# Kernel tuning notes

Measured on AMD Instinct MI355X. Metric: run time of the kernel, lower is better.

Reference implementation:

```python
import jax, jax.numpy as jnp
import numpy as np

S = 5            # num_species
B = 1_000_000    # batch (proteins)
D = 32           # input_dim == hidden_dim (hard-coded 32 in forward)
EPS = 1e-5       # torch BatchNorm1d default eps
BRANCH_WEIGHT = 0.92


def setup_inputs() -> dict:
    key = jax.random.key(0)
    ks = jax.random.split(key, 20)
    f32 = jnp.float32
    inp = {
        "network_feat": jax.random.normal(ks[0], (B, D), f32),
        "species_ids": jax.random.randint(ks[1], (B,), 0, S),
        # per-species params, stacked along species axis. Weights stored [in, out]
        # (transpose of torch nn.Linear layout) so y = x @ W + b.
        "W1": jax.random.normal(ks[2], (S, D, D), f32) * 0.1,
        "b1": jax.random.normal(ks[3], (S, D), f32) * 0.1,
        "bn1_gamma": jax.random.uniform(ks[4], (S, D), f32, 0.5, 1.5),
        "bn1_beta": jax.random.normal(ks[5], (S, D), f32) * 0.1,
        "bn1_mean": jax.random.normal(ks[6], (S, D), f32) * 0.1,
        "bn1_var": jax.random.uniform(ks[7], (S, D), f32, 0.5, 1.5),
        "W2": jax.random.normal(ks[8], (S, D, D), f32) * 0.1,
        "b2": jax.random.normal(ks[9], (S, D), f32) * 0.1,
        "bn2_gamma": jax.random.uniform(ks[10], (S, D), f32, 0.5, 1.5),
        "bn2_beta": jax.random.normal(ks[11], (S, D), f32) * 0.1,
        "bn2_mean": jax.random.normal(ks[12], (S, D), f32) * 0.1,
        "bn2_var": jax.random.uniform(ks[13], (S, D), f32, 0.5, 1.5),
        "Wsc": jax.random.normal(ks[14], (S, D, D), f32) * 0.1,
        "bsc": jax.random.normal(ks[15], (S, D), f32) * 0.1,
        "Wsh": jax.random.normal(ks[16], (D, D), f32) * 0.1,
        "bsh": jax.random.normal(ks[17], (D,), f32) * 0.1,
    }
    return inp


def _bn(h, gamma, beta, mean, var):
    # BatchNorm1d in eval mode: running-stat normalization + affine.
    return (h - mean) * jax.lax.rsqrt(var + EPS) * gamma + beta


def reference(network_feat, species_ids, W1, b1, bn1_gamma, bn1_beta, bn1_mean,
              bn1_var, W2, b2, bn2_gamma, bn2_beta, bn2_mean, bn2_var,
              Wsc, bsc, Wsh, bsh):
    # Eval mode: dropout = identity, BN uses running stats.
    # Instead of gather/scatter per species, compute each species' tiny MLP on the
    # full batch and select with the species mask (same math; dense & fusible).
    x = network_feat
    out = jnp.zeros_like(x)
    for s in range(S):  # small fixed expert count
        shortcut = x @ Wsc[s] + bsc[s]
        h = jax.nn.relu(x @ W1[s] + b1[s])
        h = _bn(h, bn1_gamma[s], bn1_beta[s], bn1_mean[s], bn1_var[s])
        h = jax.nn.relu(h @ W2[s] + b2[s] + shortcut)
        h = _bn(h, bn2_gamma[s], bn2_beta[s], bn2_mean[s], bn2_var[s])
        mask = (species_ids == s)[:, None]  # [B, 1]
        out = jnp.where(mask, h, out)
    out = jax.nn.relu(out @ Wsh + bsh)  # shared MLP (dropout inactive)
    return out * BRANCH_WEIGHT
```

## Files before the change

### kernel.cpp

```cpp
#include <hip/hip_runtime.h>


#define EPSBN 1e-5f
#define TPB 256
#define NBLKMAX 768
#define WROWS 1024
#define MAXSLOT 1184
#define MAXTILE 37

typedef __attribute__((ext_vector_type(8))) short bf16x8;
typedef __attribute__((ext_vector_type(16))) float f32x16;
typedef __attribute__((ext_vector_type(4))) unsigned u32x4;

union FU { unsigned u[4]; bf16x8 v; u32x4 q; };

static __device__ __forceinline__ unsigned pkbf(float lo, float hi) {
    unsigned r;
    asm("v_cvt_pk_bf16_f32 %0, %1, %2" : "=v"(r) : "v"(lo), "v"(hi));
    return r;
}

__global__ void k_pre(unsigned* __restrict__ wfrag, float* __restrict__ bconst,
                      const float* __restrict__ W1, const float* __restrict__ b1,
                      const float* __restrict__ g1, const float* __restrict__ be1,
                      const float* __restrict__ mu1, const float* __restrict__ va1,
                      const float* __restrict__ W2, const float* __restrict__ b2,
                      const float* __restrict__ g2, const float* __restrict__ be2,
                      const float* __restrict__ mu2, const float* __restrict__ va2,
                      const float* __restrict__ Wsc, const float* __restrict__ bsc,
                      const float* __restrict__ Wsh, const float* __restrict__ bsh) {
    if (blockIdx.x < 40) {
        const int i = blockIdx.x * 256 + threadIdx.x;
        const int p = i & 3, l = (i >> 2) & 63, c = (i >> 8) & 1;
        const int m = (i >> 9) & 3, s = i >> 11;
        const int ln = l & 31, hi = l >> 5;
        const int k0 = c * 16 + hi * 8 + 2 * p;
        float lo, hv;
        if (m == 0)      { lo = W1[s*1024 + k0*32 + ln];  hv = W1[s*1024 + (k0+1)*32 + ln]; }
        else if (m == 1) { lo = Wsc[s*1024 + k0*32 + ln]; hv = Wsc[s*1024 + (k0+1)*32 + ln]; }
        else if (m == 2) {
            float A0 = g1[s*32+k0]   * rsqrtf(va1[s*32+k0]   + EPSBN);
            float A1 = g1[s*32+k0+1] * rsqrtf(va1[s*32+k0+1] + EPSBN);
            lo = A0 * W2[s*1024 + k0*32 + ln]; hv = A1 * W2[s*1024 + (k0+1)*32 + ln];
        } else {
            float A0 = 0.92f * g2[s*32+k0]   * rsqrtf(va2[s*32+k0]   + EPSBN);
            float A1 = 0.92f * g2[s*32+k0+1] * rsqrtf(va2[s*32+k0+1] + EPSBN);
            lo = A0 * Wsh[k0*32 + ln]; hv = A1 * Wsh[(k0+1)*32 + ln];
        }
        wfrag[i] = pkbf(lo, hv);
    } else {
        for (int i = threadIdx.x; i < 480; i += 256) {
            const int reg = i & 15, hi = (i >> 4) & 1, t = i >> 5;
            const int q = t % 3, s = t / 3;
            const int r = (reg & 3) + 8 * (reg >> 2) + 4 * hi;
            float v;
            if (q == 0) v = b1[s*32 + r];
            else if (q == 1) {
                v = b2[s*32 + r] + bsc[s*32 + r];
                for (int k = 0; k < 32; ++k) {
                    float A = g1[s*32+k] * rsqrtf(va1[s*32+k] + EPSBN);
                    float C = be1[s*32+k] - mu1[s*32+k] * A;
                    v = fmaf(C, W2[s*1024 + k*32 + r], v);
                }
            } else {
                v = bsh[r];
                for (int k = 0; k < 32; ++k) {
                    float A = g2[s*32+k] * rsqrtf(va2[s*32+k] + EPSBN);
                    float C = be2[s*32+k] - mu2[s*32+k] * A;
                    v = fmaf(C, Wsh[k*32 + r], v);
                }
                v *= 0.92f;
            }
            bconst[i] = v;
        }
    }
}

static __device__ __forceinline__ void reluT(const f32x16& c, bf16x8& f0, bf16x8& f1) {
    unsigned p[8];
    #pragma unroll
    for (int i = 0; i < 8; ++i)
        p[i] = pkbf(fmaxf(c[2 * i], 0.f), fmaxf(c[2 * i + 1], 0.f));
    auto s0 = __builtin_amdgcn_permlane32_swap(p[0], p[2], false, false);
    auto s1 = __builtin_amdgcn_permlane32_swap(p[1], p[3], false, false);
    auto s2 = __builtin_amdgcn_permlane32_swap(p[4], p[6], false, false);
    auto s3 = __builtin_amdgcn_permlane32_swap(p[5], p[7], false, false);
    FU u0, u1;
    u0.u[0] = s0[0]; u0.u[1] = s1[0]; u0.u[2] = s0[1]; u0.u[3] = s1[1];
    u1.u[0] = s2[0]; u1.u[1] = s3[0]; u1.u[2] = s2[1]; u1.u[3] = s3[1];
    f0 = u0.v; f1 = u1.v;
}

struct XR { float4 a, b, c, d; };

static __device__ __forceinline__ XR ldx(const float* __restrict__ X, long ofs, int hi) {
    const float* xb = X + ofs + hi * 8;
    XR r;
    r.a = *(const float4*)(xb);
    r.b = *(const float4*)(xb + 4);
    r.c = *(const float4*)(xb + 16);
    r.d = *(const float4*)(xb + 20);
    return r;
}

static __device__ __forceinline__ void cvtx(const XR& x, bf16x8& b0, bf16x8& b1) {
    FU u0, u1;
    u0.u[0] = pkbf(x.a.x, x.a.y); u0.u[1] = pkbf(x.a.z, x.a.w);
    u0.u[2] = pkbf(x.b.x, x.b.y); u0.u[3] = pkbf(x.b.z, x.b.w);
    u1.u[0] = pkbf(x.c.x, x.c.y); u1.u[1] = pkbf(x.c.z, x.c.w);
    u1.u[2] = pkbf(x.d.x, x.d.y); u1.u[3] = pkbf(x.d.z, x.d.w);
    b0 = u0.v; b1 = u1.v;
}

static __device__ __forceinline__ void store_row(float* __restrict__ op, const f32x16& a3) {
    #pragma unroll
    for (int q = 0; q < 4; ++q) {
        float4 v;
        v.x = fmaxf(a3[4 * q + 0], 0.f);
        v.y = fmaxf(a3[4 * q + 1], 0.f);
        v.z = fmaxf(a3[4 * q + 2], 0.f);
        v.w = fmaxf(a3[4 * q + 3], 0.f);
        *(float4*)(op + q * 8) = v;
    }
}

__global__ __launch_bounds__(TPB, 3) void k_main(
    const float* __restrict__ X, const int* __restrict__ sid,
    const unsigned* __restrict__ wfrag, const float* __restrict__ bconst,
    float* __restrict__ out, int B) {
    __shared__ unsigned wlds[10240];
    __shared__ float clds[480];
    __shared__ int idxl[MAXSLOT];
    __shared__ int wq[4][4][5];
    __shared__ int tspec[MAXTILE];
    __shared__ int sgb[8];

    for (int i = threadIdx.x; i < 10240; i += TPB) wlds[i] = wfrag[i];
    for (int i = threadIdx.x; i < 480; i += TPB) clds[i] = bconst[i];

    const int tid = threadIdx.x;
    const int l   = tid & 63;
    const int ln  = l & 31;
    const int hi  = l >> 5;
    const int wav = tid >> 6;
    const unsigned long long ltmask = (1ull << l) - 1ull;

    const int nwin = (B + WROWS - 1) / WROWS;

    for (int w = blockIdx.x; w < nwin; w += gridDim.x) {
        const int wbase = w * WROWS;

        for (int i = tid; i < MAXSLOT; i += TPB) idxl[i] = -1;
        int sv[4];
        #pragma unroll
        for (int it = 0; it < 4; ++it) {
            const int row = wbase + it * TPB + tid;
            sv[it] = (row < B) ? sid[row] : -1;
            #pragma unroll
            for (int sp = 0; sp < 5; ++sp) {
                unsigned long long m = __ballot(sv[it] == sp);
                if (l == 0) wq[it][wav][sp] = (int)__popcll(m);
            }
        }
        __syncthreads();

        if (tid == 0) {
            int o = 0, tt = 0;
            for (int s = 0; s < 5; ++s) {
                int c = 0;
                for (int it = 0; it < 4; ++it)
                    for (int w2 = 0; w2 < 4; ++w2) c += wq[it][w2][s];
                sgb[s] = o;
                int nt = (c + 31) >> 5;
                for (int k = 0; k < nt; ++k) tspec[tt++] = s;
                o += nt << 5;
            }
            sgb[5] = tt;
        }
        __syncthreads();

        #pragma unroll
        for (int it = 0; it < 4; ++it) {
            const int s = sv[it];
            int rank = 0;
            #pragma unroll
            for (int sp = 0; sp < 5; ++sp) {
                unsigned long long m = __ballot(s == sp);
                if (s == sp) rank = (int)__popcll(m & ltmask);
            }
            if (s >= 0) {
                int off = sgb[s];
                for (int t2 = 0; t2 < it; ++t2)
                    #pragma unroll
                    for (int w2 = 0; w2 < 4; ++w2) off += wq[t2][w2][s];
                for (int w2 = 0; w2 < wav; ++w2) off += wq[it][w2][s];
                idxl[off + rank] = wbase + it * TPB + tid;
            }
        }
        __syncthreads();

        const int ntl = sgb[5];
        int t = wav;
        int sp = 0, id = -1;
        XR xc;
        if (t < ntl) {
            sp = __builtin_amdgcn_readfirstlane(tspec[t]);
            id = idxl[t * 32 + ln];
            xc = ldx(X, (long)(id < 0 ? 0 : id) * 32, hi);
        }
        for (; t < ntl; t += 4) {
            bf16x8 b0, b1;
            cvtx(xc, b0, b1);
            const int csp = sp, cid = id;

            const int tn = t + 4;
            if (tn < ntl) {
                sp = __builtin_amdgcn_readfirstlane(tspec[tn]);
                id = idxl[tn * 32 + ln];
                xc = ldx(X, (long)(id < 0 ? 0 : id) * 32, hi);
            }

            const unsigned* wp = wlds + csp * 2048;
            const float*    cp = clds + csp * 96;
            FU w00, w01, w10, w11, w20, w21, w30, w31;
            w00.q = *(const u32x4*)(wp + (0 * 64 + l) * 4);
            w01.q = *(const u32x4*)(wp + (1 * 64 + l) * 4);
            w10.q = *(const u32x4*)(wp + (2 * 64 + l) * 4);
            w11.q = *(const u32x4*)(wp + (3 * 64 + l) * 4);

            f32x16 a1 = *(const f32x16*)(cp + (0 * 2 + hi) * 16);
            f32x16 a2 = *(const f32x16*)(cp + (1 * 2 + hi) * 16);
            a1 = __builtin_amdgcn_mfma_f32_32x32x16_bf16(w00.v, b0, a1, 0, 0, 0);
            a2 = __builtin_amdgcn_mfma_f32_32x32x16_bf16(w10.v, b0, a2, 0, 0, 0);
            a1 = __builtin_amdgcn_mfma_f32_32x32x16_bf16(w01.v, b1, a1, 0, 0, 0);
            a2 = __builtin_amdgcn_mfma_f32_32x32x16_bf16(w11.v, b1, a2, 0, 0, 0);

            bf16x8 h0, h1;
            reluT(a1, h0, h1);
            w20.q = *(const u32x4*)(wp + (4 * 64 + l) * 4);
            w21.q = *(const u32x4*)(wp + (5 * 64 + l) * 4);
            a2 = __builtin_amdgcn_mfma_f32_32x32x16_bf16(w20.v, h0, a2, 0, 0, 0);
            a2 = __builtin_amdgcn_mfma_f32_32x32x16_bf16(w21.v, h1, a2, 0, 0, 0);

            bf16x8 g0, g1;
            reluT(a2, g0, g1);
            w30.q = *(const u32x4*)(wp + (6 * 64 + l) * 4);
            w31.q = *(const u32x4*)(wp + (7 * 64 + l) * 4);
            f32x16 a3 = *(const f32x16*)(cp + (2 * 2 + hi) * 16);
            a3 = __builtin_amdgcn_mfma_f32_32x32x16_bf16(w30.v, g0, a3, 0, 0, 0);
            a3 = __builtin_amdgcn_mfma_f32_32x32x16_bf16(w31.v, g1, a3, 0, 0, 0);

            if (cid >= 0) store_row(out + (long)cid * 32 + hi * 4, a3);
        }
        __syncthreads();
    }
}

extern "C" void kernel_launch(void* const* d_in, const int* in_sizes, int n_in,
                              void* d_out, int out_size, void* d_ws, size_t ws_size,
                              hipStream_t stream) {
    const float* X   = (const float*)d_in[0];
    const int*   sid = (const int*)d_in[1];
    const float* W1  = (const float*)d_in[2];
    const float* b1  = (const float*)d_in[3];
    const float* g1  = (const float*)d_in[4];
    const float* be1 = (const float*)d_in[5];
    const float* mu1 = (const float*)d_in[6];
    const float* va1 = (const float*)d_in[7];
    const float* W2  = (const float*)d_in[8];
    const float* b2  = (const float*)d_in[9];
    const float* g2  = (const float*)d_in[10];
    const float* be2 = (const float*)d_in[11];
    const float* mu2 = (const float*)d_in[12];
    const float* va2 = (const float*)d_in[13];
    const float* Wsc = (const float*)d_in[14];
    const float* bsc = (const float*)d_in[15];
    const float* Wsh = (const float*)d_in[16];
    const float* bsh = (const float*)d_in[17];
    float* out = (float*)d_out;
    const int B = in_sizes[1];

    unsigned* wfrag = (unsigned*)d_ws;
    float* bconst   = (float*)(wfrag + 10240);

    k_pre<<<41, 256, 0, stream>>>(wfrag, bconst,
                                  W1, b1, g1, be1, mu1, va1,
                                  W2, b2, g2, be2, mu2, va2,
                                  Wsc, bsc, Wsh, bsh);

    const int nwin = (B + WROWS - 1) / WROWS;
    const int nblocks = min(NBLKMAX, nwin);
    k_main<<<nblocks, TPB, 0, stream>>>(X, sid, wfrag, bconst, out, B);
}
```

Before: 79.52 us.

## Stage X window coalesced into swizzled LDS, read weights from global

Shrinks the per-block window from 1024 to 256 rows and loads the window's X rows with fully coalesced float4 reads, converting them to bf16 into an XOR-swizzled LDS buffer instead of gathering scattered rows per tile. Weight fragments are no longer copied into LDS but read directly from global/L2 per tile, which cuts LDS use and allows higher occupancy (launch bounds 4, up to 1024 blocks). The register prefetch pipeline across tiles is dropped, and the smaller window raises per-species padding overhead and the number of barriers per row processed.

```diff
diff --git a/kernel.cpp b/kernel.cpp
--- a/kernel.cpp
+++ b/kernel.cpp
@@ -3,10 +3,8 @@
 
 #define EPSBN 1e-5f
 #define TPB 256
-#define NBLKMAX 768
-#define WROWS 1024
-#define MAXSLOT 1184
-#define MAXTILE 37
+#define NBLKMAX 1024
+#define WIN 256
 
 typedef __attribute__((ext_vector_type(8))) short bf16x8;
 typedef __attribute__((ext_vector_type(16))) float f32x16;
@@ -91,27 +89,6 @@
     f0 = u0.v; f1 = u1.v;
 }
 
-struct XR { float4 a, b, c, d; };
-
-static __device__ __forceinline__ XR ldx(const float* __restrict__ X, long ofs, int hi) {
-    const float* xb = X + ofs + hi * 8;
-    XR r;
-    r.a = *(const float4*)(xb);
-    r.b = *(const float4*)(xb + 4);
-    r.c = *(const float4*)(xb + 16);
-    r.d = *(const float4*)(xb + 20);
-    return r;
-}
-
-static __device__ __forceinline__ void cvtx(const XR& x, bf16x8& b0, bf16x8& b1) {
-    FU u0, u1;
-    u0.u[0] = pkbf(x.a.x, x.a.y); u0.u[1] = pkbf(x.a.z, x.a.w);
-    u0.u[2] = pkbf(x.b.x, x.b.y); u0.u[3] = pkbf(x.b.z, x.b.w);
-    u1.u[0] = pkbf(x.c.x, x.c.y); u1.u[1] = pkbf(x.c.z, x.c.w);
-    u1.u[2] = pkbf(x.d.x, x.d.y); u1.u[3] = pkbf(x.d.z, x.d.w);
-    b0 = u0.v; b1 = u1.v;
-}
-
 static __device__ __forceinline__ void store_row(float* __restrict__ op, const f32x16& a3) {
     #pragma unroll
     for (int q = 0; q < 4; ++q) {
@@ -124,19 +101,16 @@
     }
 }
 
-__global__ __launch_bounds__(TPB, 3) void k_main(
+__global__ __launch_bounds__(TPB, 4) void k_main(
     const float* __restrict__ X, const int* __restrict__ sid,
     const unsigned* __restrict__ wfrag, const float* __restrict__ bconst,
     float* __restrict__ out, int B) {
-    __shared__ unsigned wlds[10240];
+    __shared__ __align__(16) unsigned char xb[16384];
     __shared__ float clds[480];
-    __shared__ int idxl[MAXSLOT];
-    __shared__ int wq[4][4][5];
-    __shared__ int tspec[MAXTILE];
+    __shared__ int idxl[416];
+    __shared__ int wq[4][5];
+    __shared__ int tspec[16];
     __shared__ int sgb[8];
-
-    for (int i = threadIdx.x; i < 10240; i += TPB) wlds[i] = wfrag[i];
-    for (int i = threadIdx.x; i < 480; i += TPB) clds[i] = bconst[i];
 
     const int tid = threadIdx.x;
     const int l   = tid & 63;
@@ -145,91 +119,85 @@
     const int wav = tid >> 6;
     const unsigned long long ltmask = (1ull << l) - 1ull;
 
-    const int nwin = (B + WROWS - 1) / WROWS;
-
+    for (int i = tid; i < 480; i += TPB) clds[i] = bconst[i];
+
+    const int nwin = (B + WIN - 1) / WIN;
     for (int w = blockIdx.x; w < nwin; w += gridDim.x) {
-        const int wbase = w * WROWS;
-
-        for (int i = tid; i < MAXSLOT; i += TPB) idxl[i] = -1;
-        int sv[4];
+        __syncthreads();
+        const int wbase = w * WIN;
+
+        const long fmax = (long)B * 32 - 8;
         #pragma unroll
-        for (int it = 0; it < 4; ++it) {
-            const int row = wbase + it * TPB + tid;
-            sv[it] = (row < B) ? sid[row] : -1;
-            #pragma unroll
-            for (int sp = 0; sp < 5; ++sp) {
-                unsigned long long m = __ballot(sv[it] == sp);
-                if (l == 0) wq[it][wav][sp] = (int)__popcll(m);
-            }
-        }
+        for (int k = 0; k < 4; ++k) {
+            long fo = (long)wbase * 32 + k * 2048 + tid * 8;
+            if (fo > fmax) fo = fmax;
+            float4 xa = *(const float4*)(X + fo);
+            float4 xc = *(const float4*)(X + fo + 4);
+            FU u;
+            u.u[0] = pkbf(xa.x, xa.y); u.u[1] = pkbf(xa.z, xa.w);
+            u.u[2] = pkbf(xc.x, xc.y); u.u[3] = pkbf(xc.z, xc.w);
+            const int row  = k * 64 + (tid >> 2);
+            const int slot = (tid & 3) ^ (row & 3);
+            *(u32x4*)(xb + row * 64 + slot * 16) = u.q;
+        }
+
+        const int myrow = wbase + tid;
+        const int s = (myrow < B) ? sid[myrow] : -1;
+        int prank = 0;
+        #pragma unroll
+        for (int sp = 0; sp < 5; ++sp) {
+            unsigned long long m = __ballot(s == sp);
+            if (l == 0) wq[wav][sp] = (int)__popcll(m);
+            if (s == sp) prank = (int)__popcll(m & ltmask);
+        }
+        for (int i = tid; i < 416; i += TPB) idxl[i] = -1;
         __syncthreads();
 
         if (tid == 0) {
             int o = 0, tt = 0;
-            for (int s = 0; s < 5; ++s) {
-                int c = 0;
-                for (int it = 0; it < 4; ++it)
-                    for (int w2 = 0; w2 < 4; ++w2) c += wq[it][w2][s];
-                sgb[s] = o;
+            for (int sp = 0; sp < 5; ++sp) {
+                int c = wq[0][sp] + wq[1][sp] + wq[2][sp] + wq[3][sp];
+                sgb[sp] = o;
                 int nt = (c + 31) >> 5;
-                for (int k = 0; k < nt; ++k) tspec[tt++] = s;
+                for (int kk = 0; kk < nt; ++kk) tspec[tt++] = sp;
                 o += nt << 5;
             }
             sgb[5] = tt;
         }
         __syncthreads();
 
-        #pragma unroll
-        for (int it = 0; it < 4; ++it) {
-            const int s = sv[it];
-            int rank = 0;
-            #pragma unroll
-            for (int sp = 0; sp < 5; ++sp) {
-                unsigned long long m = __ballot(s == sp);
-                if (s == sp) rank = (int)__popcll(m & ltmask);
-            }
-            if (s >= 0) {
-                int off = sgb[s];
-                for (int t2 = 0; t2 < it; ++t2)
-                    #pragma unroll
-                    for (int w2 = 0; w2 < 4; ++w2) off += wq[t2][w2][s];
-                for (int w2 = 0; w2 < wav; ++w2) off += wq[it][w2][s];
-                idxl[off + rank] = wbase + it * TPB + tid;
-            }
+        if (s >= 0) {
+            int off = sgb[s] + prank;
+            for (int w2 = 0; w2 < wav; ++w2) off += wq[w2][s];
+            idxl[off] = tid;
         }
         __syncthreads();
 
         const int ntl = sgb[5];
-        int t = wav;
-        int sp = 0, id = -1;
-        XR xc;
-        if (t < ntl) {
-            sp = __builtin_amdgcn_readfirstlane(tspec[t]);
-            id = idxl[t * 32 + ln];
-            xc = ldx(X, (long)(id < 0 ? 0 : id) * 32, hi);
-        }
-        for (; t < ntl; t += 4) {
-            bf16x8 b0, b1;
-            cvtx(xc, b0, b1);
-            const int csp = sp, cid = id;
-
-            const int tn = t + 4;
-            if (tn < ntl) {
-                sp = __builtin_amdgcn_readfirstlane(tspec[tn]);
-                id = idxl[tn * 32 + ln];
-                xc = ldx(X, (long)(id < 0 ? 0 : id) * 32, hi);
-            }
-
-            const unsigned* wp = wlds + csp * 2048;
-            const float*    cp = clds + csp * 96;
+        for (int t = wav; t < ntl; t += 4) {
+            const int csp = __builtin_amdgcn_readfirstlane(tspec[t]);
+            const int lid = idxl[t * 32 + ln];
+            const int r = lid < 0 ? 0 : lid;
+
+            const unsigned* wp = wfrag + csp * 2048;
             FU w00, w01, w10, w11, w20, w21, w30, w31;
             w00.q = *(const u32x4*)(wp + (0 * 64 + l) * 4);
             w01.q = *(const u32x4*)(wp + (1 * 64 + l) * 4);
             w10.q = *(const u32x4*)(wp + (2 * 64 + l) * 4);
             w11.q = *(const u32x4*)(wp + (3 * 64 + l) * 4);
-
-            f32x16 a1 = *(const f32x16*)(cp + (0 * 2 + hi) * 16);
-            f32x16 a2 = *(const f32x16*)(cp + (1 * 2 + hi) * 16);
+            w20.q = *(const u32x4*)(wp + (4 * 64 + l) * 4);
+            w21.q = *(const u32x4*)(wp + (5 * 64 + l) * 4);
+            w30.q = *(const u32x4*)(wp + (6 * 64 + l) * 4);
+            w31.q = *(const u32x4*)(wp + (7 * 64 + l) * 4);
+
+            const float* cp = clds + csp * 96;
+            f32x16 a1 = *(const f32x16*)(cp + hi * 16);
+            f32x16 a2 = *(const f32x16*)(cp + 32 + hi * 16);
+
+            const int rs = r & 3;
+            const bf16x8 b0 = *(const bf16x8*)(xb + r * 64 + ((hi ^ rs) << 4));
+            const bf16x8 b1 = *(const bf16x8*)(xb + r * 64 + (((2 + hi) ^ rs) << 4));
+
             a1 = __builtin_amdgcn_mfma_f32_32x32x16_bf16(w00.v, b0, a1, 0, 0, 0);
             a2 = __builtin_amdgcn_mfma_f32_32x32x16_bf16(w10.v, b0, a2, 0, 0, 0);
             a1 = __builtin_amdgcn_mfma_f32_32x32x16_bf16(w01.v, b1, a1, 0, 0, 0);
@@ -237,22 +205,17 @@
 
             bf16x8 h0, h1;
             reluT(a1, h0, h1);
-            w20.q = *(const u32x4*)(wp + (4 * 64 + l) * 4);
-            w21.q = *(const u32x4*)(wp + (5 * 64 + l) * 4);
             a2 = __builtin_amdgcn_mfma_f32_32x32x16_bf16(w20.v, h0, a2, 0, 0, 0);
             a2 = __builtin_amdgcn_mfma_f32_32x32x16_bf16(w21.v, h1, a2, 0, 0, 0);
 
             bf16x8 g0, g1;
             reluT(a2, g0, g1);
-            w30.q = *(const u32x4*)(wp + (6 * 64 + l) * 4);
-            w31.q = *(const u32x4*)(wp + (7 * 64 + l) * 4);
-            f32x16 a3 = *(const f32x16*)(cp + (2 * 2 + hi) * 16);
+            f32x16 a3 = *(const f32x16*)(cp + 64 + hi * 16);
             a3 = __builtin_amdgcn_mfma_f32_32x32x16_bf16(w30.v, g0, a3, 0, 0, 0);
             a3 = __builtin_amdgcn_mfma_f32_32x32x16_bf16(w31.v, g1, a3, 0, 0, 0);
 
-            if (cid >= 0) store_row(out + (long)cid * 32 + hi * 4, a3);
-        }
-        __syncthreads();
+            if (lid >= 0) store_row(out + (long)(wbase + lid) * 32 + hi * 4, a3);
+        }
     }
 }
 
@@ -288,7 +251,7 @@
                                   W2, b2, g2, be2, mu2, va2,
                                   Wsc, bsc, Wsh, bsh);
 
-    const int nwin = (B + WROWS - 1) / WROWS;
+    const int nwin = (B + WIN - 1) / WIN;
     const int nblocks = min(NBLKMAX, nwin);
     k_main<<<nblocks, TPB, 0, stream>>>(X, sid, wfrag, bconst, out, B);
 }
```

Result: faster. 71.41 us (-10.2%).
